# Performance work log

Hardware: AMD Instinct MI355X
Metric: run time of the kernel (lower is better)

Reference implementation:

```python
import jax, jax.numpy as jnp
import numpy as np

T, D, H, E, K = 4096, 1024, 2048, 8, 2  # tokens, input_size, hidden_size, num_experts, top_k


def setup_inputs() -> dict:
    key = jax.random.key(0)
    k1, k2, k3, k4, k5 = jax.random.split(key, 5)
    x = jax.random.normal(k1, (T, D), dtype=jnp.float32)
    expert_p = jax.random.uniform(k2, (T, K), dtype=jnp.float32)
    expert_idxs = jax.random.randint(k3, (T, K), 0, E, dtype=jnp.int32).astype(jnp.int64)
    # ParallelExperts weights: up-proj D -> 2H (h | gates), down-proj H -> D
    W_up = jax.random.normal(k4, (E, D, 2 * H), dtype=jnp.float32) * (D ** -0.5)
    W_down = jax.random.normal(k5, (E, H, D), dtype=jnp.float32) * (H ** -0.5)
    return {"x": x, "expert_p": expert_p, "expert_idxs": expert_idxs, "W_up": W_up, "W_down": W_down}


def reference(x, expert_p, expert_idxs, W_up, W_down):
    # x: [T, D]; expert_p/expert_idxs: [T, K]; W_up: [E, D, 2H]; W_down: [E, H, D]
    t = x.shape[0]
    e = W_up.shape[0]
    # Up projection for every expert, then GLU: out = silu(gates) * h with (h, gates) = chunk(up, 2)
    up = jnp.einsum('td,edh->teh', x, W_up)                  # [T, E, 2H]
    h, gates = jnp.split(up, 2, axis=-1)                     # each [T, E, H]
    act = jax.nn.silu(gates) * h                             # [T, E, H]
    y_all = jnp.einsum('teh,ehd->ted', act, W_down)          # [T, E, D]
    # Scatter gating weights to dense [T, E] (equivalent to sparse combine over top-k)
    dense_g = jnp.zeros((t, e), dtype=x.dtype).at[
        jnp.arange(t)[:, None], expert_idxs].add(expert_p)   # [T, E]
    y = jnp.einsum('ted,te->td', y_all, dense_g)             # [T, D]
    return y
```

## Files before the change

kernel.cpp:

```cpp
#include <hip/hip_runtime.h>
#include <hip/hip_bf16.h>
#include <stdint.h>

#define TT    4096
#define DD    1024
#define HH    2048
#define TWOH  4096
#define EE    8
#define NPAIR 8192

typedef __attribute__((ext_vector_type(8))) short bf16x8;
typedef __attribute__((ext_vector_type(4))) float f32x4;

__device__ __forceinline__ unsigned short f32_bf16(float f) {
  union { float f; unsigned int u; } v; v.f = f;
  return (unsigned short)((v.u + 0x7FFFu + ((v.u >> 16) & 1u)) >> 16);
}

__device__ __forceinline__ void gload_lds16(const unsigned short* g, unsigned short* l) {
  __builtin_amdgcn_global_load_lds(
      (const __attribute__((address_space(1))) unsigned int*)g,
      (__attribute__((address_space(3))) unsigned int*)l, 16, 0, 0);
}

__global__ void k_convert_x(const float* __restrict__ x, unsigned short* __restrict__ xb) {
  int i = blockIdx.x * blockDim.x + threadIdx.x;
  const float4* x4 = (const float4*)x;
  float4 v = x4[i];
  ushort4 o;
  o.x = f32_bf16(v.x); o.y = f32_bf16(v.y); o.z = f32_bf16(v.z); o.w = f32_bf16(v.w);
  *(ushort4*)(xb + (size_t)i * 4) = o;
}

__global__ void k_transpose64(const float* __restrict__ src, unsigned short* __restrict__ dst,
                              int R, int C) {
  __shared__ float tile[64][65];
  int e = blockIdx.z;
  const float* s = src + (size_t)e * R * C;
  unsigned short* d = dst + (size_t)e * R * C;
  int c0 = blockIdx.x * 64, r0 = blockIdx.y * 64;
  int t = threadIdx.x;
  int lr = t >> 4;
  int lc = (t & 15) * 4;
#pragma unroll
  for (int i = 0; i < 4; i++) {
    int r = i * 16 + lr;
    float4 v = *(const float4*)(s + (size_t)(r0 + r) * C + c0 + lc);
    tile[r][lc + 0] = v.x; tile[r][lc + 1] = v.y;
    tile[r][lc + 2] = v.z; tile[r][lc + 3] = v.w;
  }
  __syncthreads();
  int sc = t >> 4;
  int sr = (t & 15) * 4;
#pragma unroll
  for (int i = 0; i < 4; i++) {
    int c = i * 16 + sc;
    ushort4 o;
    o.x = f32_bf16(tile[sr + 0][c]);
    o.y = f32_bf16(tile[sr + 1][c]);
    o.z = f32_bf16(tile[sr + 2][c]);
    o.w = f32_bf16(tile[sr + 3][c]);
    *(ushort4*)(d + (size_t)(c0 + c) * R + r0 + sr) = o;
  }
}

__global__ void k_route(const int* __restrict__ idx, const float* __restrict__ p,
                        int* __restrict__ tok, float* __restrict__ pw,
                        int* __restrict__ inv, int* __restrict__ se) {
  __shared__ int cnt[EE];
  __shared__ int base[EE];
  __shared__ int cur[EE];
  int t = threadIdx.x;
  if (t < EE) cnt[t] = 0;
  __syncthreads();
  for (int i = t; i < NPAIR; i += blockDim.x) atomicAdd(&cnt[idx[i]], 1);
  __syncthreads();
  if (t == 0) {
    int acc = 0;
    for (int e = 0; e < EE; e++) { base[e] = acc; cur[e] = acc; acc += cnt[e]; }
  }
  __syncthreads();
  for (int i = t; i < NPAIR; i += blockDim.x) {
    int e = idx[i];
    int pos = atomicAdd(&cur[e], 1);
    tok[pos] = i >> 1;
    pw[pos]  = p[i];
    inv[i]   = pos;
  }
  if (t < EE) { se[t] = base[t]; se[EE + t] = base[t] + cnt[t]; }
}

__launch_bounds__(256)
__global__ void k_gemm1(const unsigned short* __restrict__ xb,
                        const unsigned short* __restrict__ wup,
                        const int* __restrict__ tok,
                        const int* __restrict__ se,
                        unsigned short* __restrict__ act) {
  const int e = blockIdx.z;
  const int start = se[e], end = se[EE + e];
  const int row_base = start + blockIdx.y * 128;
  if (row_base >= end) return;
  const int c0 = blockIdx.x * 64;

  __shared__ __align__(16) unsigned short Als[128 * 64];
  __shared__ __align__(16) unsigned short Bls[128 * 64];

  const int t = threadIdx.x;
  const int lane = t & 63;
  const int w = t >> 6;
  const int wr = w >> 1, wc = w & 1;

  const int srow = t >> 3;
  const int ls = (t & 7) ^ (srow & 7);
  const unsigned short* wup_e = wup + (size_t)e * TWOH * DD;

  const unsigned short* srcA[4];
  const unsigned short* srcB[4];
  unsigned short* dstA[4];
  unsigned short* dstB[4];
#pragma unroll
  for (int i = 0; i < 4; i++) {
    int row = i * 32 + srow;
    int ridx = row_base + row; if (ridx > end - 1) ridx = end - 1;
    srcA[i] = xb + (size_t)tok[ridx] * DD + ls * 8;
    int nrow = (row < 64) ? (c0 + row) : (HH + c0 + (row - 64));
    srcB[i] = wup_e + (size_t)nrow * DD + ls * 8;
    dstA[i] = Als + ((size_t)i * 256 + t) * 8;
    dstB[i] = Bls + ((size_t)i * 256 + t) * 8;
  }

  f32x4 acc_h[4][2], acc_g[4][2];
#pragma unroll
  for (int m = 0; m < 4; m++)
#pragma unroll
    for (int n = 0; n < 2; n++) {
      acc_h[m][n] = (f32x4){0.f, 0.f, 0.f, 0.f};
      acc_g[m][n] = (f32x4){0.f, 0.f, 0.f, 0.f};
    }

  for (int kt = 0; kt < DD / 64; kt++) {
#pragma unroll
    for (int i = 0; i < 4; i++) gload_lds16(srcA[i], dstA[i]);
#pragma unroll
    for (int i = 0; i < 4; i++) gload_lds16(srcB[i], dstB[i]);
#pragma unroll
    for (int i = 0; i < 4; i++) { srcA[i] += 64; srcB[i] += 64; }
    __syncthreads();

#pragma unroll
    for (int ksub = 0; ksub < 2; ksub++) {
      const int kslot = ksub * 4 + (lane >> 4);
      bf16x8 a[4], bh[2], bg[2];
#pragma unroll
      for (int m = 0; m < 4; m++) {
        int r = wr * 64 + m * 16 + (lane & 15);
        a[m] = *(const bf16x8*)(Als + r * 64 + ((kslot ^ (r & 7)) * 8));
      }
#pragma unroll
      for (int n = 0; n < 2; n++) {
        int rh = wc * 32 + n * 16 + (lane & 15);
        bh[n] = *(const bf16x8*)(Bls + rh * 64 + ((kslot ^ (rh & 7)) * 8));
        int rg = 64 + rh;
        bg[n] = *(const bf16x8*)(Bls + rg * 64 + ((kslot ^ (rg & 7)) * 8));
      }
#pragma unroll
      for (int m = 0; m < 4; m++)
#pragma unroll
        for (int n = 0; n < 2; n++) {
          acc_h[m][n] = __builtin_amdgcn_mfma_f32_16x16x32_bf16(a[m], bh[n], acc_h[m][n], 0, 0, 0);
          acc_g[m][n] = __builtin_amdgcn_mfma_f32_16x16x32_bf16(a[m], bg[n], acc_g[m][n], 0, 0, 0);
        }
    }
    __syncthreads();
  }

#pragma unroll
  for (int m = 0; m < 4; m++) {
#pragma unroll
    for (int j = 0; j < 4; j++) {
      int rloc = wr * 64 + m * 16 + ((lane >> 4) * 4) + j;
      int rg = row_base + rloc;
      if (rg < end) {
#pragma unroll
        for (int n = 0; n < 2; n++) {
          float h = acc_h[m][n][j];
          float g = acc_g[m][n][j];
          float sv = (g / (1.f + __expf(-g))) * h;
          act[(size_t)rg * HH + (c0 + wc * 32 + n * 16 + (lane & 15))] = f32_bf16(sv);
        }
      }
    }
  }
}

__launch_bounds__(256)
__global__ void k_gemm2(const unsigned short* __restrict__ act,
                        const unsigned short* __restrict__ wdn,
                        const float* __restrict__ pw,
                        const int* __restrict__ se,
                        float* __restrict__ yp) {
  const int e = blockIdx.z;
  const int start = se[e], end = se[EE + e];
  const int row_base = start + blockIdx.y * 128;
  if (row_base >= end) return;
  const int c0 = blockIdx.x * 128;

  __shared__ __align__(16) unsigned short Als[128 * 64];
  __shared__ __align__(16) unsigned short Bls[128 * 64];

  const int t = threadIdx.x;
  const int lane = t & 63;
  const int w = t >> 6;
  const int wr = w >> 1, wc = w & 1;

  const int srow = t >> 3;
  const int ls = (t & 7) ^ (srow & 7);
  const unsigned short* wdn_e = wdn + (size_t)e * DD * HH;

  const unsigned short* srcA[4];
  const unsigned short* srcB[4];
  unsigned short* dstA[4];
  unsigned short* dstB[4];
#pragma unroll
  for (int i = 0; i < 4; i++) {
    int row = i * 32 + srow;
    int ridx = row_base + row; if (ridx > end - 1) ridx = end - 1;
    srcA[i] = act + (size_t)ridx * HH + ls * 8;
    srcB[i] = wdn_e + (size_t)(c0 + row) * HH + ls * 8;
    dstA[i] = Als + ((size_t)i * 256 + t) * 8;
    dstB[i] = Bls + ((size_t)i * 256 + t) * 8;
  }

  f32x4 acc[4][4];
#pragma unroll
  for (int m = 0; m < 4; m++)
#pragma unroll
    for (int n = 0; n < 4; n++) acc[m][n] = (f32x4){0.f, 0.f, 0.f, 0.f};

  for (int kt = 0; kt < HH / 64; kt++) {
#pragma unroll
    for (int i = 0; i < 4; i++) gload_lds16(srcA[i], dstA[i]);
#pragma unroll
    for (int i = 0; i < 4; i++) gload_lds16(srcB[i], dstB[i]);
#pragma unroll
    for (int i = 0; i < 4; i++) { srcA[i] += 64; srcB[i] += 64; }
    __syncthreads();

#pragma unroll
    for (int ksub = 0; ksub < 2; ksub++) {
      const int kslot = ksub * 4 + (lane >> 4);
      bf16x8 a[4], b[4];
#pragma unroll
      for (int m = 0; m < 4; m++) {
        int r = wr * 64 + m * 16 + (lane & 15);
        a[m] = *(const bf16x8*)(Als + r * 64 + ((kslot ^ (r & 7)) * 8));
      }
#pragma unroll
      for (int n = 0; n < 4; n++) {
        int rb = wc * 64 + n * 16 + (lane & 15);
        b[n] = *(const bf16x8*)(Bls + rb * 64 + ((kslot ^ (rb & 7)) * 8));
      }
#pragma unroll
      for (int m = 0; m < 4; m++)
#pragma unroll
        for (int n = 0; n < 4; n++)
          acc[m][n] = __builtin_amdgcn_mfma_f32_16x16x32_bf16(a[m], b[n], acc[m][n], 0, 0, 0);
    }
    __syncthreads();
  }

#pragma unroll
  for (int m = 0; m < 4; m++) {
#pragma unroll
    for (int j = 0; j < 4; j++) {
      int rloc = wr * 64 + m * 16 + ((lane >> 4) * 4) + j;
      int rg = row_base + rloc;
      if (rg < end) {
        float p = pw[rg];
#pragma unroll
        for (int n = 0; n < 4; n++) {
          int col = c0 + wc * 64 + n * 16 + (lane & 15);
          yp[(size_t)rg * DD + col] = p * acc[m][n][j];
        }
      }
    }
  }
}

__global__ void k_combine(const float* __restrict__ yp, const int* __restrict__ inv,
                          float* __restrict__ y) {
  int i = blockIdx.x * blockDim.x + threadIdx.x;
  int tk = i >> 8;
  int d4 = i & 255;
  const float4* yp4 = (const float4*)yp;
  float4 a = yp4[(size_t)inv[2 * tk] * (DD / 4) + d4];
  float4 b = yp4[(size_t)inv[2 * tk + 1] * (DD / 4) + d4];
  float4 o = make_float4(a.x + b.x, a.y + b.y, a.z + b.z, a.w + b.w);
  ((float4*)y)[i] = o;
}

extern "C" void kernel_launch(void* const* d_in, const int* in_sizes, int n_in,
                              void* d_out, int out_size, void* d_ws, size_t ws_size,
                              hipStream_t stream) {
  const float* x        = (const float*)d_in[0];
  const float* expert_p = (const float*)d_in[1];
  const int*   expert_i = (const int*)d_in[2];
  const float* W_up     = (const float*)d_in[3];
  const float* W_down   = (const float*)d_in[4];
  float* y = (float*)d_out;

  char* ws = (char*)d_ws;
  const size_t OFF_XB  = 0;
  const size_t OFF_WUP = 8388608;
  const size_t OFF_WDN = 75497472;
  const size_t OFF_ACT = 109051904;
  const size_t OFF_TOK = 142606336;
  const size_t OFF_PW  = 142639104;
  const size_t OFF_INV = 142671872;
  const size_t OFF_SE  = 142704640;

  unsigned short* xb   = (unsigned short*)(ws + OFF_XB);
  unsigned short* wupb = (unsigned short*)(ws + OFF_WUP);
  unsigned short* wdnb = (unsigned short*)(ws + OFF_WDN);
  unsigned short* actb = (unsigned short*)(ws + OFF_ACT);
  float* yp  = (float*)(ws + OFF_WUP);
  int*   tok = (int*)(ws + OFF_TOK);
  float* pw  = (float*)(ws + OFF_PW);
  int*   inv = (int*)(ws + OFF_INV);
  int*   se  = (int*)(ws + OFF_SE);

  k_convert_x<<<(TT * DD / 4 + 255) / 256, 256, 0, stream>>>(x, xb);
  k_transpose64<<<dim3(TWOH / 64, DD / 64, EE), 256, 0, stream>>>(W_up, wupb, DD, TWOH);
  k_transpose64<<<dim3(DD / 64, HH / 64, EE), 256, 0, stream>>>(W_down, wdnb, HH, DD);
  k_route<<<1, 1024, 0, stream>>>(expert_i, expert_p, tok, pw, inv, se);
  k_gemm1<<<dim3(HH / 64, NPAIR / 128, EE), 256, 0, stream>>>(xb, wupb, tok, se, actb);
  k_gemm2<<<dim3(DD / 128, NPAIR / 128, EE), 256, 0, stream>>>(actb, wdnb, pw, se, yp);
  k_combine<<<(TT * DD / 4) / 256, 256, 0, stream>>>(yp, inv, y);
}
```

Baseline: 471.6 us.

## Double-buffer LDS in both expert GEMMs and narrow gemm2 column tile

Both grouped GEMM kernels now keep two LDS buffers and issue the async global-to-LDS loads for the next K tile before computing on the current one, so loads overlap MFMA work. This also removes one barrier per iteration. gemm2's column tile drops from 128 to 64, doubling its grid so more blocks can run concurrently. The cost is more LDS per block, which may limit occupancy, and more redundant A-tile loads in gemm2.

```diff
diff --git a/kernel.cpp b/kernel.cpp
--- a/kernel.cpp
+++ b/kernel.cpp
@@ -102,8 +102,8 @@
   if (row_base >= end) return;
   const int c0 = blockIdx.x * 64;
 
-  __shared__ __align__(16) unsigned short Als[128 * 64];
-  __shared__ __align__(16) unsigned short Bls[128 * 64];
+  __shared__ __align__(16) unsigned short Als[2 * 128 * 64];
+  __shared__ __align__(16) unsigned short Bls[2 * 128 * 64];
 
   const int t = threadIdx.x;
   const int lane = t & 63;
@@ -116,8 +116,6 @@
 
   const unsigned short* srcA[4];
   const unsigned short* srcB[4];
-  unsigned short* dstA[4];
-  unsigned short* dstB[4];
 #pragma unroll
   for (int i = 0; i < 4; i++) {
     int row = i * 32 + srow;
@@ -125,9 +123,16 @@
     srcA[i] = xb + (size_t)tok[ridx] * DD + ls * 8;
     int nrow = (row < 64) ? (c0 + row) : (HH + c0 + (row - 64));
     srcB[i] = wup_e + (size_t)nrow * DD + ls * 8;
-    dstA[i] = Als + ((size_t)i * 256 + t) * 8;
-    dstB[i] = Bls + ((size_t)i * 256 + t) * 8;
-  }
+  }
+
+  auto stage = [&](int buf) {
+    unsigned short* aB = Als + buf * (128 * 64);
+    unsigned short* bB = Bls + buf * (128 * 64);
+#pragma unroll
+    for (int i = 0; i < 4; i++) gload_lds16(srcA[i], aB + (size_t)(i * 256 + t) * 8);
+#pragma unroll
+    for (int i = 0; i < 4; i++) gload_lds16(srcB[i], bB + (size_t)(i * 256 + t) * 8);
+  };
 
   f32x4 acc_h[4][2], acc_g[4][2];
 #pragma unroll
@@ -138,15 +143,17 @@
       acc_g[m][n] = (f32x4){0.f, 0.f, 0.f, 0.f};
     }
 
+  stage(0);
+  __syncthreads();
+  int cur = 0;
+
   for (int kt = 0; kt < DD / 64; kt++) {
 #pragma unroll
-    for (int i = 0; i < 4; i++) gload_lds16(srcA[i], dstA[i]);
-#pragma unroll
-    for (int i = 0; i < 4; i++) gload_lds16(srcB[i], dstB[i]);
-#pragma unroll
     for (int i = 0; i < 4; i++) { srcA[i] += 64; srcB[i] += 64; }
-    __syncthreads();
-
+    if (kt + 1 < DD / 64) stage(cur ^ 1);
+
+    const unsigned short* aT = Als + cur * (128 * 64);
+    const unsigned short* bT = Bls + cur * (128 * 64);
 #pragma unroll
     for (int ksub = 0; ksub < 2; ksub++) {
       const int kslot = ksub * 4 + (lane >> 4);
@@ -154,14 +161,14 @@
 #pragma unroll
       for (int m = 0; m < 4; m++) {
         int r = wr * 64 + m * 16 + (lane & 15);
-        a[m] = *(const bf16x8*)(Als + r * 64 + ((kslot ^ (r & 7)) * 8));
+        a[m] = *(const bf16x8*)(aT + r * 64 + ((kslot ^ (r & 7)) * 8));
       }
 #pragma unroll
       for (int n = 0; n < 2; n++) {
         int rh = wc * 32 + n * 16 + (lane & 15);
-        bh[n] = *(const bf16x8*)(Bls + rh * 64 + ((kslot ^ (rh & 7)) * 8));
+        bh[n] = *(const bf16x8*)(bT + rh * 64 + ((kslot ^ (rh & 7)) * 8));
         int rg = 64 + rh;
-        bg[n] = *(const bf16x8*)(Bls + rg * 64 + ((kslot ^ (rg & 7)) * 8));
+        bg[n] = *(const bf16x8*)(bT + rg * 64 + ((kslot ^ (rg & 7)) * 8));
       }
 #pragma unroll
       for (int m = 0; m < 4; m++)
@@ -172,6 +179,7 @@
         }
     }
     __syncthreads();
+    cur ^= 1;
   }
 
 #pragma unroll
@@ -203,10 +211,10 @@
   const int start = se[e], end = se[EE + e];
   const int row_base = start + blockIdx.y * 128;
   if (row_base >= end) return;
-  const int c0 = blockIdx.x * 128;
-
-  __shared__ __align__(16) unsigned short Als[128 * 64];
-  __shared__ __align__(16) unsigned short Bls[128 * 64];
+  const int c0 = blockIdx.x * 64;
+
+  __shared__ __align__(16) unsigned short Als[2 * 128 * 64];
+  __shared__ __align__(16) unsigned short Bls[2 * 64 * 64];
 
   const int t = threadIdx.x;
   const int lane = t & 63;
@@ -218,55 +226,69 @@
   const unsigned short* wdn_e = wdn + (size_t)e * DD * HH;
 
   const unsigned short* srcA[4];
-  const unsigned short* srcB[4];
-  unsigned short* dstA[4];
-  unsigned short* dstB[4];
+  const unsigned short* srcB[2];
 #pragma unroll
   for (int i = 0; i < 4; i++) {
     int row = i * 32 + srow;
     int ridx = row_base + row; if (ridx > end - 1) ridx = end - 1;
     srcA[i] = act + (size_t)ridx * HH + ls * 8;
+  }
+#pragma unroll
+  for (int i = 0; i < 2; i++) {
+    int row = i * 32 + srow;
     srcB[i] = wdn_e + (size_t)(c0 + row) * HH + ls * 8;
-    dstA[i] = Als + ((size_t)i * 256 + t) * 8;
-    dstB[i] = Bls + ((size_t)i * 256 + t) * 8;
-  }
-
-  f32x4 acc[4][4];
+  }
+
+  auto stage = [&](int buf) {
+    unsigned short* aB = Als + buf * (128 * 64);
+    unsigned short* bB = Bls + buf * (64 * 64);
+#pragma unroll
+    for (int i = 0; i < 4; i++) gload_lds16(srcA[i], aB + (size_t)(i * 256 + t) * 8);
+#pragma unroll
+    for (int i = 0; i < 2; i++) gload_lds16(srcB[i], bB + (size_t)(i * 256 + t) * 8);
+  };
+
+  f32x4 acc[4][2];
 #pragma unroll
   for (int m = 0; m < 4; m++)
 #pragma unroll
-    for (int n = 0; n < 4; n++) acc[m][n] = (f32x4){0.f, 0.f, 0.f, 0.f};
+    for (int n = 0; n < 2; n++) acc[m][n] = (f32x4){0.f, 0.f, 0.f, 0.f};
+
+  stage(0);
+  __syncthreads();
+  int cur = 0;
 
   for (int kt = 0; kt < HH / 64; kt++) {
 #pragma unroll
-    for (int i = 0; i < 4; i++) gload_lds16(srcA[i], dstA[i]);
-#pragma unroll
-    for (int i = 0; i < 4; i++) gload_lds16(srcB[i], dstB[i]);
-#pragma unroll
-    for (int i = 0; i < 4; i++) { srcA[i] += 64; srcB[i] += 64; }
-    __syncthreads();
-
+    for (int i = 0; i < 4; i++) srcA[i] += 64;
+#pragma unroll
+    for (int i = 0; i < 2; i++) srcB[i] += 64;
+    if (kt + 1 < HH / 64) stage(cur ^ 1);
+
+    const unsigned short* aT = Als + cur * (128 * 64);
+    const unsigned short* bT = Bls + cur * (64 * 64);
 #pragma unroll
     for (int ksub = 0; ksub < 2; ksub++) {
       const int kslot = ksub * 4 + (lane >> 4);
-      bf16x8 a[4], b[4];
+      bf16x8 a[4], b[2];
 #pragma unroll
       for (int m = 0; m < 4; m++) {
         int r = wr * 64 + m * 16 + (lane & 15);
-        a[m] = *(const bf16x8*)(Als + r * 64 + ((kslot ^ (r & 7)) * 8));
-      }
-#pragma unroll
-      for (int n = 0; n < 4; n++) {
-        int rb = wc * 64 + n * 16 + (lane & 15);
-        b[n] = *(const bf16x8*)(Bls + rb * 64 + ((kslot ^ (rb & 7)) * 8));
+        a[m] = *(const bf16x8*)(aT + r * 64 + ((kslot ^ (r & 7)) * 8));
+      }
+#pragma unroll
+      for (int n = 0; n < 2; n++) {
+        int rb = wc * 32 + n * 16 + (lane & 15);
+        b[n] = *(const bf16x8*)(bT + rb * 64 + ((kslot ^ (rb & 7)) * 8));
       }
 #pragma unroll
       for (int m = 0; m < 4; m++)
 #pragma unroll
-        for (int n = 0; n < 4; n++)
+        for (int n = 0; n < 2; n++)
           acc[m][n] = __builtin_amdgcn_mfma_f32_16x16x32_bf16(a[m], b[n], acc[m][n], 0, 0, 0);
     }
     __syncthreads();
+    cur ^= 1;
   }
 
 #pragma unroll
@@ -278,8 +300,8 @@
       if (rg < end) {
         float p = pw[rg];
 #pragma unroll
-        for (int n = 0; n < 4; n++) {
-          int col = c0 + wc * 64 + n * 16 + (lane & 15);
+        for (int n = 0; n < 2; n++) {
+          int col = c0 + wc * 32 + n * 16 + (lane & 15);
           yp[(size_t)rg * DD + col] = p * acc[m][n][j];
         }
       }
@@ -334,6 +356,6 @@
   k_transpose64<<<dim3(DD / 64, HH / 64, EE), 256, 0, stream>>>(W_down, wdnb, HH, DD);
   k_route<<<1, 1024, 0, stream>>>(expert_i, expert_p, tok, pw, inv, se);
   k_gemm1<<<dim3(HH / 64, NPAIR / 128, EE), 256, 0, stream>>>(xb, wupb, tok, se, actb);
-  k_gemm2<<<dim3(DD / 128, NPAIR / 128, EE), 256, 0, stream>>>(actb, wdnb, pw, se, yp);
+  k_gemm2<<<dim3(DD / 64, NPAIR / 128, EE), 256, 0, stream>>>(actb, wdnb, pw, se, yp);
   k_combine<<<(TT * DD / 4) / 256, 256, 0, stream>>>(yp, inv, y);
 }
```

Result: no change. 473.4 us (+0.4%).
